# Kernel tuning notes

Hardware: AMD Instinct MI355X
Metric: run time of the kernel (lower is better)

Reference implementation:

```python
import jax, jax.numpy as jnp
import numpy as np

NUM_HEADS = 16
HEAD_DIM = 128  # d_out // num_heads
D_IN = 2048
D_OUT = 2048
B = 2
T = 2048
W_SCALE = 0.02  # keep softmax logits in a sane range


def setup_inputs() -> dict:
    key = jax.random.key(0)
    ks = jax.random.split(key, 6)
    x = jax.random.normal(ks[0], (B, T, D_IN), dtype=jnp.float32)
    Wq = jax.random.normal(ks[1], (D_OUT, D_IN), dtype=jnp.float32) * W_SCALE
    Wk = jax.random.normal(ks[2], (HEAD_DIM, D_IN), dtype=jnp.float32) * W_SCALE
    Wv = jax.random.normal(ks[3], (HEAD_DIM, D_IN), dtype=jnp.float32) * W_SCALE
    Wo = jax.random.normal(ks[4], (D_OUT, D_OUT), dtype=jnp.float32) * W_SCALE
    bo = jnp.zeros((D_OUT,), dtype=jnp.float32)
    return {"x": x, "Wq": Wq, "Wk": Wk, "Wv": Wv, "Wo": Wo, "bo": bo}


def reference(x, Wq, Wk, Wv, Wo, bo):
    b, t, _ = x.shape
    # projections (torch nn.Linear: y = x @ W.T)
    q = jnp.einsum('btd,ed->bte', x, Wq).reshape(b, t, NUM_HEADS, HEAD_DIM)
    q = q.transpose(0, 2, 1, 3)                      # [b, H, T, hd]
    k = jnp.einsum('btd,ed->bte', x, Wk)             # [b, T, hd] single KV head
    v = jnp.einsum('btd,ed->bte', x, Wv)             # [b, T, hd]
    # MQA: single K/V head broadcast across all query heads
    scale = 1.0 / jnp.sqrt(jnp.float32(HEAD_DIM))
    scores = jnp.einsum('bhqd,bkd->bhqk', q, k) * scale  # [b, H, T, T]
    # NOTE: the original module computes a causal mask but never applies it,
    # so attention is unmasked (faithful to source).
    w = jax.nn.softmax(scores, axis=-1)
    ctx = jnp.einsum('bhqk,bkd->bhqd', w, v)         # [b, H, T, hd]
    ctx = ctx.transpose(0, 2, 1, 3).reshape(b, t, D_OUT)
    return jnp.einsum('btd,ed->bte', ctx, Wo) + bo
```

## Files before the change

kernel.cpp:

```cpp
#include <hip/hip_runtime.h>

typedef unsigned short u16;
typedef unsigned int   u32;
typedef __bf16 bf16x8 __attribute__((ext_vector_type(8)));
typedef float  f32x4  __attribute__((ext_vector_type(4)));
typedef u32    u32x2  __attribute__((ext_vector_type(2)));

constexpr int TB   = 2;
constexpr int TT   = 2048;
constexpr int DIN  = 2048;
constexpr int DOUT = 2048;
constexpr int NH   = 16;
constexpr int HD   = 128;
constexpr int MR   = TB * TT;
constexpr int NQKV = DOUT + 2 * HD;

constexpr float QSC = 0.08838834764831845f * 1.4426950408889634f;

__device__ __forceinline__ u16 f2b(float f) {
  return __builtin_bit_cast(u16, (__bf16)f);
}

__global__ __launch_bounds__(256) void k_cast_all(const float* __restrict__ x,
                                                  const float* __restrict__ wq,
                                                  const float* __restrict__ wk,
                                                  const float* __restrict__ wv,
                                                  const float* __restrict__ wo,
                                                  u16* __restrict__ xb,
                                                  u16* __restrict__ wqkv,
                                                  u16* __restrict__ wob) {
  int bid = blockIdx.x;
  const float* s; u16* d; int base;
  if (bid < 8192)       { s = x;  d = xb;   base = bid; }
  else if (bid < 12288) { s = wq; d = wqkv; base = bid - 8192; }
  else if (bid < 12544) { s = wk; d = wqkv + (size_t)DOUT * DIN;        base = bid - 12288; }
  else if (bid < 12800) { s = wv; d = wqkv + (size_t)(DOUT + HD) * DIN; base = bid - 12544; }
  else                  { s = wo; d = wob;  base = bid - 12800; }
  int i = (base * 256 + threadIdx.x) * 4;
  float4 v = *(const float4*)(s + i);
  ushort4 o;
  o.x = f2b(v.x); o.y = f2b(v.y); o.z = f2b(v.z); o.w = f2b(v.w);
  *(ushort4*)(d + i) = o;
}

__device__ __forceinline__ void async16(const u16* g, u16* l) {
  __builtin_amdgcn_global_load_lds((const __attribute__((address_space(1))) void*)g,
                                   (__attribute__((address_space(3))) void*)l,
                                   16, 0, 0);
}

#define GPH2(KK)                                                                   \
  {                                                                                \
    bf16x8 af[4], bfv[4];                                                          \
    const char* baA = (const char*)&lA[cur][0];                                    \
    const char* baB = (const char*)&lB[cur][0];                                    \
    const int cso = (((KK) * 4 + kq) ^ sw) << 4;                                   \
    _Pragma("unroll")                                                              \
    for (int mm = 0; mm < 4; ++mm)                                                 \
      af[mm] = *(const bf16x8*)(baA + (wr * 64 + mm * 16 + r16) * 128 + cso);      \
    _Pragma("unroll")                                                              \
    for (int n = 0; n < 4; ++n)                                                    \
      bfv[n] = *(const bf16x8*)(baB + (wc * 64 + n * 16 + r16) * 128 + cso);       \
    __builtin_amdgcn_s_barrier();                                                  \
    __builtin_amdgcn_s_setprio(1);                                                 \
    _Pragma("unroll")                                                              \
    for (int mm = 0; mm < 4; ++mm)                                                 \
      _Pragma("unroll")                                                            \
      for (int n = 0; n < 4; ++n)                                                  \
        acc[mm][n] = __builtin_amdgcn_mfma_f32_16x16x32_bf16(                      \
            af[mm], bfv[n], acc[mm][n], 0, 0, 0);                                  \
    __builtin_amdgcn_s_setprio(0);                                                 \
    __builtin_amdgcn_s_barrier();                                                  \
  }

template<bool F32OUT>
__global__ __launch_bounds__(512, 2) void k_gemm8(const u16* __restrict__ A,
                                                  const u16* __restrict__ Bm,
                                                  void* __restrict__ Cv,
                                                  const float* __restrict__ bias,
                                                  int M, int N, int K) {
  __shared__ u16 lA[2][128 * 64];
  __shared__ u16 lB[2][256 * 64];
  const int tid = threadIdx.x;
  const int w = tid >> 6, l = tid & 63;
  const int wr = w >> 2, wc = w & 3;
  const int r16 = l & 15, kq = l >> 4;
  const int sw = r16 & 7;

  int nwg = gridDim.x * gridDim.y;
  int wg = blockIdx.y * gridDim.x + blockIdx.x;
  if ((nwg & 7) == 0) wg = (wg & 7) * (nwg >> 3) + (wg >> 3);
  const int rowS = (wg / gridDim.x) * 128, colS = (wg % gridDim.x) * 256;

  auto stageA = [&](int buf, int k0) {
#pragma unroll
    for (int i = 0; i < 2; ++i) {
      int e = i * 512 + tid;
      int row = e >> 3;
      int gc = ((e & 7) ^ (row & 7)) * 8;
      async16(A + (size_t)(rowS + row) * K + k0 + gc, &lA[buf][e * 8]);
    }
  };
  auto stageB = [&](int buf, int k0) {
#pragma unroll
    for (int i = 0; i < 4; ++i) {
      int e = i * 512 + tid;
      int row = e >> 3;
      int gc = ((e & 7) ^ (row & 7)) * 8;
      async16(Bm + (size_t)(colS + row) * K + k0 + gc, &lB[buf][e * 8]);
    }
  };

  f32x4 acc[4][4] = {};

  stageA(0, 0);
  stageB(0, 0);

  const int NT = K >> 6;
  int cur = 0;
  for (int t = 0; t < NT; ++t) {
    const bool pre = (t + 1 < NT);
    if (pre) {
      stageA(cur ^ 1, (t + 1) << 6);
      stageB(cur ^ 1, (t + 1) << 6);
      asm volatile("s_waitcnt vmcnt(6)" ::: "memory");
    } else {
      asm volatile("s_waitcnt vmcnt(0)" ::: "memory");
    }
    __builtin_amdgcn_s_barrier();

    GPH2(0);
    GPH2(1);
    cur ^= 1;
  }

#pragma unroll
  for (int m = 0; m < 4; ++m)
#pragma unroll
    for (int n = 0; n < 4; ++n)
#pragma unroll
      for (int j = 0; j < 4; ++j) {
        int r = rowS + wr * 64 + m * 16 + kq * 4 + j;
        int c = colS + wc * 64 + n * 16 + r16;
        if constexpr (F32OUT) {
          ((float*)Cv)[(size_t)r * N + c] = acc[m][n][j] + bias[c];
        } else {
          float v = acc[m][n][j];
          if (c < DOUT) v *= QSC;
          ((u16*)Cv)[(size_t)r * N + c] = f2b(v);
        }
      }
}

__global__ __launch_bounds__(256) void k_transpose_v(const u16* __restrict__ qkv,
                                                     u16* __restrict__ vtg) {
  __shared__ u16 tile[64 * 136];
  const int blk = blockIdx.x;
  const int b = blk / (TT / 64), t0 = (blk % (TT / 64)) * 64;
  const int tid = threadIdx.x;
#pragma unroll
  for (int i = 0; i < 4; ++i) {
    int e = i * 256 + tid;
    int row = e >> 4, col = (e & 15) * 8;
    *(uint4*)&tile[row * 136 + col] =
        *(const uint4*)(qkv + (size_t)(b * TT + t0 + row) * NQKV + DOUT + HD + col);
  }
  __syncthreads();
#pragma unroll
  for (int i = 0; i < 4; ++i) {
    int e = i * 256 + tid;
    int d = e >> 3, tc = (e & 7) * 8;
    u16 tmp[8];
#pragma unroll
    for (int j = 0; j < 8; ++j) tmp[j] = tile[(tc + j) * 136 + d];
    *(uint4*)(vtg + ((size_t)b * HD + d) * TT + t0 + tc) = *(uint4*)tmp;
  }
}

#define KT_IDX(r, c) ((r) * 128 + ((c) ^ (((r) & 7) << 3)))
#define VT_IDX(r, c) ((r) * 64 + ((c) ^ (((r) & 7) << 3)))

__global__ __launch_bounds__(512) void k_attn(const u16* __restrict__ qkv,
                                              const u16* __restrict__ vtg,
                                              u16* __restrict__ ctxg) {
  __shared__ u16 Kt[2][64 * 128];
  __shared__ u16 Vt[2][128 * 64];
  __shared__ u16 Pt[8][16 * 40];

  const int qt = blockIdx.x, h = blockIdx.y, b = blockIdx.z;
  const int tid = threadIdx.x, w = tid >> 6, l = tid & 63;
  const int r16 = l & 15, kq = l >> 4;
  const int q0 = qt * 128 + w * 16;
  const size_t rowbase = (size_t)b * TT;

  bf16x8 qf[4];
  const u16* qrow = qkv + (rowbase + q0 + r16) * NQKV + h * HD + kq * 8;
#pragma unroll
  for (int kk = 0; kk < 4; ++kk) qf[kk] = *(const bf16x8*)(qrow + kk * 32);

  const int krow0 = tid >> 4, kcol = (tid & 15) * 8;
  const int vrow0 = tid >> 3, vcol = (tid & 7) * 8;
  const u16* kglob = qkv + (rowbase)*NQKV + DOUT;
  const u16* vglob = vtg + (size_t)b * HD * TT;

  uint4 kr0, kr1, vr0, vr1;
  auto load_tiles = [&](int kv0) {
    const u16* kb = kglob + (size_t)kv0 * NQKV;
    kr0 = *(const uint4*)(kb + (size_t)krow0 * NQKV + kcol);
    kr1 = *(const uint4*)(kb + (size_t)(krow0 + 32) * NQKV + kcol);
    const u16* vb = vglob + kv0;
    vr0 = *(const uint4*)(vb + (size_t)vrow0 * TT + vcol);
    vr1 = *(const uint4*)(vb + (size_t)(vrow0 + 64) * TT + vcol);
  };
  auto write_tiles = [&](int buf) {
    *(uint4*)&Kt[buf][KT_IDX(krow0, kcol)]      = kr0;
    *(uint4*)&Kt[buf][KT_IDX(krow0 + 32, kcol)] = kr1;
    *(uint4*)&Vt[buf][VT_IDX(vrow0, vcol)]      = vr0;
    *(uint4*)&Vt[buf][VT_IDX(vrow0 + 64, vcol)] = vr1;
  };

  f32x4 ctx[8] = {};
  float l_run = 0.0f;

  load_tiles(0);
  write_tiles(0);
  __syncthreads();

  for (int t = 0; t < TT / 64; ++t) {
    const int cur = t & 1;
    if (t < TT / 64 - 1) load_tiles((t + 1) * 64);

    f32x4 s[4] = {};
#pragma unroll
    for (int n = 0; n < 4; ++n) {
      bf16x8 kf[4];
#pragma unroll
      for (int kk = 0; kk < 4; ++kk)
        kf[kk] = *(const bf16x8*)&Kt[cur][KT_IDX(n * 16 + r16, kk * 32 + kq * 8)];
      __builtin_amdgcn_s_setprio(1);
#pragma unroll
      for (int kk = 0; kk < 4; ++kk)
        s[n] = __builtin_amdgcn_mfma_f32_16x16x32_bf16(kf[kk], qf[kk], s[n], 0, 0, 0);
      __builtin_amdgcn_s_setprio(0);
    }

    float rsum = 0.0f;
    float p[4][4];
#pragma unroll
    for (int n = 0; n < 4; ++n)
#pragma unroll
      for (int j = 0; j < 4; ++j) {
        p[n][j] = exp2f(s[n][j]);
        rsum += p[n][j];
      }
    rsum += __shfl_xor(rsum, 16);
    rsum += __shfl_xor(rsum, 32);
    l_run += rsum;

    u32 pk[4][2];
#pragma unroll
    for (int n = 0; n < 4; ++n) {
      pk[n][0] = (u32)f2b(p[n][0]) | ((u32)f2b(p[n][1]) << 16);
      pk[n][1] = (u32)f2b(p[n][2]) | ((u32)f2b(p[n][3]) << 16);
    }

    u16* pw = Pt[w];
#pragma unroll
    for (int hh = 0; hh < 2; ++hh) {
      u32x2 w0, w1;
      w0[0] = pk[2 * hh][0];     w0[1] = pk[2 * hh][1];
      w1[0] = pk[2 * hh + 1][0]; w1[1] = pk[2 * hh + 1][1];
      *(u32x2*)&pw[r16 * 40 + kq * 4]      = w0;
      *(u32x2*)&pw[r16 * 40 + 16 + kq * 4] = w1;
      bf16x8 pf = *(const bf16x8*)&pw[r16 * 40 + kq * 8];
      __builtin_amdgcn_s_setprio(1);
#pragma unroll
      for (int f = 0; f < 8; ++f) {
        bf16x8 vf = *(const bf16x8*)&Vt[cur][VT_IDX(f * 16 + r16, hh * 32 + kq * 8)];
        ctx[f] = __builtin_amdgcn_mfma_f32_16x16x32_bf16(vf, pf, ctx[f], 0, 0, 0);
      }
      __builtin_amdgcn_s_setprio(0);
    }

    if (t < TT / 64 - 1) write_tiles(cur ^ 1);
    __syncthreads();
  }

  const float inv = 1.0f / l_run;
  u16* crow = ctxg + (rowbase + q0 + r16) * DOUT + h * HD + kq * 4;
#pragma unroll
  for (int f = 0; f < 8; ++f) {
    u32x2 o;
    o[0] = (u32)f2b(ctx[f][0] * inv) | ((u32)f2b(ctx[f][1] * inv) << 16);
    o[1] = (u32)f2b(ctx[f][2] * inv) | ((u32)f2b(ctx[f][3] * inv) << 16);
    *(u32x2*)(crow + f * 16) = o;
  }
}

extern "C" void kernel_launch(void* const* d_in, const int* in_sizes, int n_in,
                              void* d_out, int out_size, void* d_ws, size_t ws_size,
                              hipStream_t stream) {
  const float* x  = (const float*)d_in[0];
  const float* Wq = (const float*)d_in[1];
  const float* Wk = (const float*)d_in[2];
  const float* Wv = (const float*)d_in[3];
  const float* Wo = (const float*)d_in[4];
  const float* bo = (const float*)d_in[5];
  float* out = (float*)d_out;

  char* ws = (char*)d_ws;
  u16* xb   = (u16*)(ws + 0);
  u16* wqkv = (u16*)(ws + 16777216);
  u16* wo   = (u16*)(ws + 26214400);
  u16* qkv  = (u16*)(ws + 34603008);
  u16* vtg  = (u16*)(ws + 53477376);
  u16* ctx  = (u16*)(ws + 54525952);

  k_cast_all<<<16896, 256, 0, stream>>>(x, Wq, Wk, Wv, Wo, xb, wqkv, wo);

  k_gemm8<false><<<dim3(NQKV / 256, MR / 128), 512, 0, stream>>>(
      xb, wqkv, (void*)qkv, nullptr, MR, NQKV, DIN);

  k_transpose_v<<<TB * TT / 64, 256, 0, stream>>>(qkv, vtg);

  k_attn<<<dim3(TT / 128, NH, TB), 512, 0, stream>>>(qkv, vtg, ctx);

  k_gemm8<true><<<dim3(DOUT / 256, MR / 128), 512, 0, stream>>>(
      ctx, wo, (void*)out, bo, MR, DOUT, DOUT);
}
```

Baseline: 350.7 us.

## Triple-buffer GEMM LDS staging and interleave async loads with MFMA phases

The bf16 GEMM kernel moves from double-buffered to triple-buffered LDS, prefetching two K-tiles ahead. Global-to-LDS async loads are split across the two MFMA sub-phases so that issue overlaps with compute, and the vmcnt wait moves to the end of each iteration. LDS use grows to 144KB per block and the occupancy hint of 2 blocks per CU is dropped, which likely leaves one resident workgroup per CU.

New measurement: 317.1 us. 9.6% less time.

```diff
diff --git a/kernel.cpp b/kernel.cpp
--- a/kernel.cpp
+++ b/kernel.cpp
@@ -49,38 +49,40 @@
                                    16, 0, 0);
 }
 
-#define GPH2(KK)                                                                   \
-  {                                                                                \
-    bf16x8 af[4], bfv[4];                                                          \
-    const char* baA = (const char*)&lA[cur][0];                                    \
-    const char* baB = (const char*)&lB[cur][0];                                    \
-    const int cso = (((KK) * 4 + kq) ^ sw) << 4;                                   \
-    _Pragma("unroll")                                                              \
-    for (int mm = 0; mm < 4; ++mm)                                                 \
-      af[mm] = *(const bf16x8*)(baA + (wr * 64 + mm * 16 + r16) * 128 + cso);      \
-    _Pragma("unroll")                                                              \
-    for (int n = 0; n < 4; ++n)                                                    \
-      bfv[n] = *(const bf16x8*)(baB + (wc * 64 + n * 16 + r16) * 128 + cso);       \
-    __builtin_amdgcn_s_barrier();                                                  \
-    __builtin_amdgcn_s_setprio(1);                                                 \
-    _Pragma("unroll")                                                              \
-    for (int mm = 0; mm < 4; ++mm)                                                 \
-      _Pragma("unroll")                                                            \
-      for (int n = 0; n < 4; ++n)                                                  \
-        acc[mm][n] = __builtin_amdgcn_mfma_f32_16x16x32_bf16(                      \
-            af[mm], bfv[n], acc[mm][n], 0, 0, 0);                                  \
-    __builtin_amdgcn_s_setprio(0);                                                 \
-    __builtin_amdgcn_s_barrier();                                                  \
+#define GPH3(SUB, BUFI, STAGE_STMT, WAIT_STMT)                                 \
+  {                                                                            \
+    bf16x8 af[4], bfv[4];                                                      \
+    const char* baA = (const char*)&lA[BUFI][0];                               \
+    const char* baB = (const char*)&lB[BUFI][0];                               \
+    const int cso = (((SUB) * 4 + kq) ^ sw) << 4;                              \
+    _Pragma("unroll")                                                          \
+    for (int mm = 0; mm < 4; ++mm)                                             \
+      af[mm] = *(const bf16x8*)(baA + (wr * 64 + mm * 16 + r16) * 128 + cso);  \
+    _Pragma("unroll")                                                          \
+    for (int n = 0; n < 4; ++n)                                                \
+      bfv[n] = *(const bf16x8*)(baB + (wc * 64 + n * 16 + r16) * 128 + cso);   \
+    STAGE_STMT;                                                                \
+    __builtin_amdgcn_s_barrier();                                              \
+    __builtin_amdgcn_s_setprio(1);                                             \
+    _Pragma("unroll")                                                          \
+    for (int mm = 0; mm < 4; ++mm)                                             \
+      _Pragma("unroll")                                                        \
+      for (int n = 0; n < 4; ++n)                                              \
+        acc[mm][n] = __builtin_amdgcn_mfma_f32_16x16x32_bf16(                  \
+            af[mm], bfv[n], acc[mm][n], 0, 0, 0);                              \
+    __builtin_amdgcn_s_setprio(0);                                             \
+    WAIT_STMT;                                                                 \
+    __builtin_amdgcn_s_barrier();                                              \
   }
 
 template<bool F32OUT>
-__global__ __launch_bounds__(512, 2) void k_gemm8(const u16* __restrict__ A,
-                                                  const u16* __restrict__ Bm,
-                                                  void* __restrict__ Cv,
-                                                  const float* __restrict__ bias,
-                                                  int M, int N, int K) {
-  __shared__ u16 lA[2][128 * 64];
-  __shared__ u16 lB[2][256 * 64];
+__global__ __launch_bounds__(512) void k_gemm8(const u16* __restrict__ A,
+                                               const u16* __restrict__ Bm,
+                                               void* __restrict__ Cv,
+                                               const float* __restrict__ bias,
+                                               int M, int N, int K) {
+  __shared__ u16 lA[3][128 * 64];
+  __shared__ u16 lB[3][256 * 64];
   const int tid = threadIdx.x;
   const int w = tid >> 6, l = tid & 63;
   const int wr = w >> 2, wc = w & 3;
@@ -92,7 +94,7 @@
   if ((nwg & 7) == 0) wg = (wg & 7) * (nwg >> 3) + (wg >> 3);
   const int rowS = (wg / gridDim.x) * 128, colS = (wg % gridDim.x) * 256;
 
-  auto stageA = [&](int buf, int k0) {
+  auto stageA2 = [&](int buf, int k0) {
 #pragma unroll
     for (int i = 0; i < 2; ++i) {
       int e = i * 512 + tid;
@@ -101,9 +103,10 @@
       async16(A + (size_t)(rowS + row) * K + k0 + gc, &lA[buf][e * 8]);
     }
   };
-  auto stageB = [&](int buf, int k0) {
+  auto stageB = [&](int buf, int k0, int i0, int i1) {
 #pragma unroll
     for (int i = 0; i < 4; ++i) {
+      if (i < i0 || i >= i1) continue;
       int e = i * 512 + tid;
       int row = e >> 3;
       int gc = ((e & 7) ^ (row & 7)) * 8;
@@ -113,25 +116,31 @@
 
   f32x4 acc[4][4] = {};
 
-  stageA(0, 0);
-  stageB(0, 0);
+  stageA2(0, 0);
+  stageB(0, 0, 0, 4);
+  stageA2(1, 64);
+  stageB(1, 64, 0, 4);
+  asm volatile("s_waitcnt vmcnt(6)" ::: "memory");
+  __builtin_amdgcn_s_barrier();
 
   const int NT = K >> 6;
-  int cur = 0;
   for (int t = 0; t < NT; ++t) {
-    const bool pre = (t + 1 < NT);
-    if (pre) {
-      stageA(cur ^ 1, (t + 1) << 6);
-      stageB(cur ^ 1, (t + 1) << 6);
-      asm volatile("s_waitcnt vmcnt(6)" ::: "memory");
-    } else {
-      asm volatile("s_waitcnt vmcnt(0)" ::: "memory");
-    }
-    __builtin_amdgcn_s_barrier();
-
-    GPH2(0);
-    GPH2(1);
-    cur ^= 1;
+    const int bi = t % 3;
+    const int sb = (t + 2) % 3;
+    const bool st = (t + 2 < NT);
+    const int k2 = (t + 2) << 6;
+
+    GPH3(0, bi,
+         { if (st) { stageA2(sb, k2); stageB(sb, k2, 0, 1); } },
+         {});
+    GPH3(1, bi,
+         { if (st) { stageB(sb, k2, 1, 4); } },
+         {
+           if (t + 1 < NT) {
+             if (st) asm volatile("s_waitcnt vmcnt(6)" ::: "memory");
+             else    asm volatile("s_waitcnt vmcnt(0)" ::: "memory");
+           }
+         });
   }
 
 #pragma unroll
```
